# Optimization experiments

Measured on AMD Instinct MI355X. Metric: run time of the kernel, lower is better.

The kernel has to match this reference:

```python
import math
import jax, jax.numpy as jnp
import numpy as np

jax.config.update("jax_enable_x64", True)

P_PRIME = 1000003            # prime modulus; p-1 = 2*3*166667
N_FACTORS = (2, 3, 166667)   # prime factors of p-1 (for primitive-root search)
B, NPATCH, L, K, DIM = 4, 784, 9, 16, 28  # batch, patches/sample, patch len, kernels, map dim


def _modpow(base, exp, p, nbits=21):
    """Vectorized modular exponentiation (square-and-multiply), int64, exponents < 2^nbits."""
    shape = jnp.broadcast_shapes(jnp.shape(base), jnp.shape(exp))
    b0 = jnp.broadcast_to(jnp.asarray(base, jnp.int64) % p, shape)
    e = jnp.broadcast_to(jnp.asarray(exp, jnp.int64), shape)
    def body(i, c):
        res, b = c
        res = jnp.where(((e >> i) & 1) == 1, (res * b) % p, res)
        return (res, (b * b) % p)
    res, _ = jax.lax.fori_loop(0, nbits, body, (jnp.ones(shape, jnp.int64), b0))
    return res


def _decrypt_ips(ct0, cts, y, sk_y, g, p):
    """IPFE decrypt + BSGS discrete log. ct0:[B,P] cts:[B,P,L] y:[K,L] sk_y:[K] -> signed ip [K,B,P]."""
    n = p - 1
    powed = _modpow(cts[None], jnp.mod(y, n)[:, None, None, :], p)   # [K,B,P,L]
    num = powed[..., 0]
    for i in range(1, L):                                            # fixed small L=9
        num = (num * powed[..., i]) % p
    denom = _modpow(ct0[None], jnp.mod(sk_y, n)[:, None, None], p)   # [K,B,P]
    val = (num * _modpow(denom, p - 2, p)) % p                       # = g^{<x,y>} mod p (Fermat inverse)
    # baby-step giant-step over group order n
    m = math.isqrt(n - 1) + 1
    n_giant = -(-n // m)
    baby = _modpow(jnp.int64(g), jnp.arange(m, dtype=jnp.int64), p)  # g^j, j in [0,m)
    order = jnp.argsort(baby)
    sb = baby[order]
    ginv_m = _modpow(jnp.int64(g), jnp.int64((n - m) % n), p)        # g^{-m}
    pt = _modpow(ginv_m, jnp.arange(n_giant, dtype=jnp.int64), p)    # g^{-m*i}
    gamma = (val.reshape(-1)[:, None] * pt[None, :]) % p             # [T, n_giant] giant steps
    pos = jnp.clip(jnp.searchsorted(sb, gamma), 0, m - 1)
    hit = sb[pos] == gamma
    cand = jnp.arange(n_giant, dtype=jnp.int64)[None, :] * m + order[pos]
    ip = jnp.min(jnp.where(hit, cand, n), axis=1)                    # unique match: ip = i*m + j
    ip = jnp.where(ip > n // 2, ip - n, ip)                          # signed representative
    return ip.reshape(K, ct0.shape[0], ct0.shape[1])


def _bn(x, g_, b_, m_, v_):
    s = g_ * jax.lax.rsqrt(v_ + 1e-5)
    return (x - m_[None, :, None, None]) * s[None, :, None, None] + b_[None, :, None, None]


def _conv(x, w, b):
    o = jax.lax.conv_general_dilated(x, w, (1, 1), ((1, 1), (1, 1)),
                                     dimension_numbers=("NCHW", "OIHW", "NCHW"))
    return o + b[None, :, None, None]


def _pool(x):
    return jax.lax.reduce_window(x, jnp.array(-jnp.inf, x.dtype), jax.lax.max,
                                 (1, 1, 2, 2), (1, 1, 2, 2), "VALID")


def _forward(ct0, cts, y, sk_y, bias1, bn1_g, bn1_b, bn1_m, bn1_v,
             conv2_w, conv2_b, bn2_g, bn2_b, bn2_m, bn2_v,
             conv3_w, conv3_b, bn3_g, bn3_b, bn3_m, bn3_v,
             fc1_w, fc1_b, fc2_w, fc2_b, g, p):
    ip = _decrypt_ips(ct0, cts, y, sk_y, g, p)                       # [K,B,P] int64
    maps = ip.astype(jnp.float32) / 10000.0 + bias1[:, None, None]   # dequantize + conv1 bias
    feat = jnp.transpose(maps, (1, 0, 2)).reshape(-1, K, DIM, DIM)   # [B,16,28,28]
    feat = _pool(jax.nn.relu(_bn(feat, bn1_g, bn1_b, bn1_m, bn1_v)))
    feat = _pool(jax.nn.relu(_bn(_conv(feat, conv2_w, conv2_b), bn2_g, bn2_b, bn2_m, bn2_v)))
    feat = _pool(jax.nn.relu(_bn(_conv(feat, conv3_w, conv3_b), bn3_g, bn3_b, bn3_m, bn3_v)))
    flat = feat.reshape(feat.shape[0], -1)                           # [B,576]
    h = jax.nn.relu(flat @ fc1_w.T + fc1_b)                          # dropout = identity (eval mode)
    return h @ fc2_w.T + fc2_b                                       # [B,10]


def setup_inputs():
    rng = np.random.default_rng(0)
    p, n = P_PRIME, P_PRIME - 1
    assert all(p % d for d in range(2, math.isqrt(p) + 1))           # p prime
    g = next(gg for gg in range(2, 200)
             if all(pow(gg, n // q, p) != 1 for q in N_FACTORS))      # primitive root mod p
    s = rng.integers(1, n, size=L)                                    # master secret
    pk = [pow(g, int(si), p) for si in s]
    y = rng.integers(-50, 51, size=(K, L)).astype(np.int64)          # round(w*10000)
    x = rng.integers(0, 21, size=(B, NPATCH, L))                     # quantized patch values
    r = rng.integers(1, n, size=(B, NPATCH))
    gx = [pow(g, t, p) for t in range(21)]
    ct0 = np.zeros((B, NPATCH), dtype=np.int64)
    cts = np.zeros((B, NPATCH, L), dtype=np.int64)
    for b in range(B):
        for j in range(NPATCH):
            rr = int(r[b, j])
            ct0[b, j] = pow(g, rr, p)
            for i in range(L):
                cts[b, j, i] = pow(pk[i], rr, p) * gx[x[b, j, i]] % p
    sk_y = np.array([sum(int(s[i]) * int(y[k, i]) for i in range(L)) % n
                     for k in range(K)], dtype=np.int64)
    f32 = lambda a: jnp.asarray(a, jnp.float32)
    def rn(*sh):
        return f32(rng.standard_normal(sh) * 0.1)
    def bnp(c):
        return (f32(1.0 + 0.1 * rng.standard_normal(c)), rn(c), rn(c), f32(rng.random(c) + 0.5))
    bn1_g, bn1_b, bn1_m, bn1_v = bnp(16)
    bn2_g, bn2_b, bn2_m, bn2_v = bnp(32)
    bn3_g, bn3_b, bn3_m, bn3_v = bnp(64)
    return dict(ct0=jnp.asarray(ct0), cts=jnp.asarray(cts),
                y=jnp.asarray(y), sk_y=jnp.asarray(sk_y), bias1=rn(K),
                bn1_g=bn1_g, bn1_b=bn1_b, bn1_m=bn1_m, bn1_v=bn1_v,
                conv2_w=rn(32, 16, 3, 3), conv2_b=rn(32),
                bn2_g=bn2_g, bn2_b=bn2_b, bn2_m=bn2_m, bn2_v=bn2_v,
                conv3_w=rn(64, 32, 3, 3), conv3_b=rn(64),
                bn3_g=bn3_g, bn3_b=bn3_b, bn3_m=bn3_m, bn3_v=bn3_v,
                fc1_w=rn(128, 576), fc1_b=rn(128),
                fc2_w=rn(10, 128), fc2_b=rn(10), g=g, p=p)


def reference(ct0, cts, y, sk_y, bias1, bn1_g, bn1_b, bn1_m, bn1_v,
              conv2_w, conv2_b, bn2_g, bn2_b, bn2_m, bn2_v,
              conv3_w, conv3_b, bn3_g, bn3_b, bn3_m, bn3_v,
              fc1_w, fc1_b, fc2_w, fc2_b, g, p):
    return _forward(ct0, cts, y, sk_y, bias1, bn1_g, bn1_b, bn1_m, bn1_v,
                    conv2_w, conv2_b, bn2_g, bn2_b, bn2_m, bn2_v,
                    conv3_w, conv3_b, bn3_g, bn3_b, bn3_m, bn3_v,
                    fc1_w, fc1_b, fc2_w, fc2_b, g, p)
```

## Files before the change

kernel.cpp:

```cpp
#include <hip/hip_runtime.h>
#include <stdint.h>

#define PRIME 1000003u
#define NORD  1000002u
#define KCH   16
#define BATCH 4
#define NPATCH 784
#define LLEN  9
#define IPMAX 9000
#define TBLN  (2*IPMAX+1)
#define NDEC  (KCH*BATCH*NPATCH)
#define NBLK  196

__device__ __forceinline__ uint32_t mmul(uint32_t a, uint32_t b) {
    uint64_t t = (uint64_t)a * (uint64_t)b;
    uint32_t q = (uint32_t)((t * 2199016ull) >> 41);
    uint32_t r = (uint32_t)t - q * PRIME;
    return (r >= PRIME) ? r - PRIME : r;
}

__device__ __forceinline__ uint32_t mpow(uint32_t base, uint32_t exp) {
    uint32_t r = 1u, b = base;
    while (exp) {
        if (exp & 1u) r = mmul(r, b);
        b = mmul(b, b);
        exp >>= 1;
    }
    return r;
}

__device__ __forceinline__ void cstore(float* p, float v) {
    __hip_atomic_store(p, v, __ATOMIC_RELAXED, __HIP_MEMORY_SCOPE_AGENT);
}
__device__ __forceinline__ float cload(const float* p) {
    return __hip_atomic_load(p, __ATOMIC_RELAXED, __HIP_MEMORY_SCOPE_AGENT);
}

__device__ __forceinline__ void arrive(unsigned* ctr) {
    __syncthreads();
    if (threadIdx.x == 0)
        __hip_atomic_fetch_add(ctr, 1u, __ATOMIC_RELAXED, __HIP_MEMORY_SCOPE_AGENT);
}
__device__ __forceinline__ void wait_ctr(unsigned* ctr, unsigned target) {
    if (threadIdx.x == 0)
        while (__hip_atomic_load(ctr, __ATOMIC_RELAXED, __HIP_MEMORY_SCOPE_AGENT) < target)
            __builtin_amdgcn_s_sleep(2);
    __syncthreads();
}

__global__ void build_table(const int* __restrict__ g_in, int16_t* __restrict__ table,
                            unsigned* __restrict__ ctr) {
    int e = blockIdx.x * blockDim.x + threadIdx.x;
    if (e >= TBLN) return;
    if (e == 0)
        __hip_atomic_store(ctr, 0u, __ATOMIC_RELAXED, __HIP_MEMORY_SCOPE_AGENT);
    int es = e - IPMAX;
    uint32_t exp = (es >= 0) ? (uint32_t)es : (uint32_t)(es + (int)NORD);
    table[mpow((uint32_t)g_in[0], exp)] = (int16_t)es;
}

__global__ void __launch_bounds__(256) fused(
    const int* __restrict__ ct0, const int* __restrict__ cts,
    const int* __restrict__ y, const int* __restrict__ sk_y,
    const float* __restrict__ bias1,
    const float* __restrict__ bn1_g, const float* __restrict__ bn1_b,
    const float* __restrict__ bn1_m, const float* __restrict__ bn1_v,
    const float* __restrict__ conv2_w, const float* __restrict__ conv2_b,
    const float* __restrict__ bn2_g, const float* __restrict__ bn2_b,
    const float* __restrict__ bn2_m, const float* __restrict__ bn2_v,
    const float* __restrict__ conv3_w, const float* __restrict__ conv3_b,
    const float* __restrict__ bn3_g, const float* __restrict__ bn3_b,
    const float* __restrict__ bn3_m, const float* __restrict__ bn3_v,
    const float* __restrict__ fc1_w, const float* __restrict__ fc1_b,
    const float* __restrict__ fc2_w, const float* __restrict__ fc2_b,
    const int16_t* __restrict__ table,
    float* __restrict__ featr, float* __restrict__ s2g, float* __restrict__ s3g,
    float* __restrict__ out, unsigned* __restrict__ ctr) {

    __shared__ union {
        struct { float s1p[16][16][16]; float w[144]; float co[196]; } c2;
        struct { float s2p[32][9][9];  float w[4][288]; float co[4][49]; } c3;
        struct { float s3[576]; float h[128]; } fc;
    } sm;

    const int bid = blockIdx.x;
    const int tid = threadIdx.x;

    {
        int gtid = bid * 256 + tid;
        int k = __builtin_amdgcn_readfirstlane(gtid / (BATCH * NPATCH));
        int r = gtid % (BATCH * NPATCH);
        int b = r / NPATCH;
        int j = r % NPATCH;

        const int* crow = cts + ((b * NPATCH) + j) * LLEN;
        const int* yrow = y + k * LLEN;

        uint32_t c[LLEN];
        int yv[LLEN];
#pragma unroll
        for (int i = 0; i < LLEN; i++) {
            yv[i] = yrow[i];
            c[i]  = (uint32_t)crow[i];
        }

        uint32_t accp = 1u, accn = 1u;
#pragma unroll
        for (int bit = 5; bit >= 0; bit--) {
            accp = mmul(accp, accp);
            accn = mmul(accn, accn);
#pragma unroll
            for (int i = 0; i < LLEN; i++) {
                int yi = yv[i];
                int ay = (yi > 0) ? yi : -yi;
                if ((ay >> bit) & 1) {
                    if (yi > 0) accp = mmul(accp, c[i]);
                    else        accn = mmul(accn, c[i]);
                }
            }
        }

        uint32_t den = mpow((uint32_t)ct0[b * NPATCH + j], (uint32_t)sk_y[k]);
        den = mmul(den, accn);
        uint32_t val = mmul(accp, mpow(den, PRIME - 2u));

        int ip = (int)table[val];

        float sc = bn1_g[k] * rsqrtf(bn1_v[k] + 1e-5f);
        float shf = (bias1[k] - bn1_m[k]) * sc + bn1_b[k];
        float v_ = fmaf((float)ip, sc * 1e-4f, shf);
        cstore(&featr[((b * KCH) + k) * NPATCH + j], fmaxf(v_, 0.0f));
    }

    arrive(ctr);
    if (bid >= 128) return;
    wait_ctr(ctr, NBLK);

    {
        const int b  = bid >> 5;
        const int oc = bid & 31;

        for (int i = tid; i < 16 * 16 * 16; i += 256)
            ((float*)sm.c2.s1p)[i] = 0.0f;
        if (tid < 144) sm.c2.w[tid] = conv2_w[oc * 144 + tid];
        __syncthreads();
        for (int i = tid; i < 16 * 196; i += 256) {
            int ic = i / 196, pos = i % 196;
            int yy = pos / 14, xx = pos % 14;
            const float* fp = featr + ((b * 16 + ic) * 784) + (2 * yy) * 28 + 2 * xx;
            sm.c2.s1p[ic][yy + 1][xx + 1] =
                fmaxf(fmaxf(cload(fp + 0), cload(fp + 1)),
                      fmaxf(cload(fp + 28), cload(fp + 29)));
        }
        __syncthreads();

        if (tid < 196) {
            int oh = tid / 14, ow = tid % 14;
            float a0 = 0.0f, a1 = 0.0f, a2 = 0.0f;
#pragma unroll
            for (int ic = 0; ic < 16; ic++) {
                const float* wp = &sm.c2.w[ic * 9];
                const float* sp = &sm.c2.s1p[ic][oh][ow];
                a0 = fmaf(sp[0],  wp[0], fmaf(sp[1],  wp[1], fmaf(sp[2],  wp[2], a0)));
                a1 = fmaf(sp[16], wp[3], fmaf(sp[17], wp[4], fmaf(sp[18], wp[5], a1)));
                a2 = fmaf(sp[32], wp[6], fmaf(sp[33], wp[7], fmaf(sp[34], wp[8], a2)));
            }
            float sc = bn2_g[oc] * rsqrtf(bn2_v[oc] + 1e-5f);
            float shf = bn2_b[oc] - bn2_m[oc] * sc;
            sm.c2.co[tid] = fmaxf((a0 + a1 + a2 + conv2_b[oc]) * sc + shf, 0.0f);
        }
        __syncthreads();

        if (tid < 49) {
            int oh = tid / 7, ow = tid % 7;
            const float* c0 = &sm.c2.co[(2 * oh) * 14 + 2 * ow];
            cstore(&s2g[((b * 32 + oc) * 49) + tid],
                   fmaxf(fmaxf(c0[0], c0[1]), fmaxf(c0[14], c0[15])));
        }
    }

    arrive(ctr);
    if (bid >= 64) return;
    wait_ctr(ctr, NBLK + 128);

    {
        const int b = bid >> 4, ocg = bid & 15;

        for (int i = tid; i < 32 * 81; i += 256)
            ((float*)sm.c3.s2p)[i] = 0.0f;
        for (int i = tid; i < 4 * 288; i += 256) {
            int w2 = i / 288, rr = i % 288;
            sm.c3.w[w2][rr] = conv3_w[(ocg * 4 + w2) * 288 + rr];
        }
        __syncthreads();
        for (int i = tid; i < 32 * 49; i += 256) {
            int ic = i / 49, pos = i % 49;
            sm.c3.s2p[ic][pos / 7 + 1][pos % 7 + 1] = cload(&s2g[((b * 32 + ic) * 49) + pos]);
        }
        __syncthreads();

        const int wid = tid >> 6, lane = tid & 63;
        if (lane < 49) {
            int oh = lane / 7, ow = lane % 7;
            float a0 = 0.0f, a1 = 0.0f, a2 = 0.0f;
#pragma unroll
            for (int ic = 0; ic < 32; ic++) {
                const float* wp = &sm.c3.w[wid][ic * 9];
                const float* sp = &sm.c3.s2p[ic][oh][ow];
                a0 = fmaf(sp[0],  wp[0], fmaf(sp[1],  wp[1], fmaf(sp[2],  wp[2], a0)));
                a1 = fmaf(sp[9],  wp[3], fmaf(sp[10], wp[4], fmaf(sp[11], wp[5], a1)));
                a2 = fmaf(sp[18], wp[6], fmaf(sp[19], wp[7], fmaf(sp[20], wp[8], a2)));
            }
            int oc = ocg * 4 + wid;
            float sc = bn3_g[oc] * rsqrtf(bn3_v[oc] + 1e-5f);
            float shf = bn3_b[oc] - bn3_m[oc] * sc;
            sm.c3.co[wid][lane] = fmaxf((a0 + a1 + a2 + conv3_b[oc]) * sc + shf, 0.0f);
        }
        __syncthreads();

        if (tid < 36) {
            int w2 = tid / 9, p = tid % 9;
            int oh = p / 3, ow = p % 3;
            const float* c0 = &sm.c3.co[w2][(2 * oh) * 7 + 2 * ow];
            cstore(&s3g[b * 576 + (ocg * 4 + w2) * 9 + p],
                   fmaxf(fmaxf(c0[0], c0[1]), fmaxf(c0[7], c0[8])));
        }
    }

    arrive(ctr);
    if (bid >= BATCH) return;
    wait_ctr(ctr, NBLK + 128 + 64);

    {
        const int b = bid;
        for (int i = tid; i < 576; i += 256) sm.fc.s3[i] = cload(&s3g[b * 576 + i]);
        __syncthreads();

        const int wid = tid >> 6, lane = tid & 63;
        for (int oo = 0; oo < 32; oo++) {
            int o = wid * 32 + oo;
            const float* w = fc1_w + o * 576;
            float acc = 0.0f;
#pragma unroll
            for (int jj = 0; jj < 9; jj++)
                acc = fmaf(sm.fc.s3[jj * 64 + lane], w[jj * 64 + lane], acc);
#pragma unroll
            for (int off = 32; off; off >>= 1) acc += __shfl_down(acc, off);
            if (lane == 0) sm.fc.h[o] = fmaxf(acc + fc1_b[o], 0.0f);
        }
        __syncthreads();

        for (int o = wid; o < 10; o += 4) {
            const float* w = fc2_w + o * 128;
            float acc = fmaf(sm.fc.h[lane], w[lane], 0.0f);
            acc = fmaf(sm.fc.h[64 + lane], w[64 + lane], acc);
#pragma unroll
            for (int off = 32; off; off >>= 1) acc += __shfl_down(acc, off);
            if (lane == 0) out[b * 10 + o] = acc + fc2_b[o];
        }
    }
}

extern "C" void kernel_launch(void* const* d_in, const int* in_sizes, int n_in,
                              void* d_out, int out_size, void* d_ws, size_t ws_size,
                              hipStream_t stream) {
    const int*   ct0    = (const int*)d_in[0];
    const int*   cts    = (const int*)d_in[1];
    const int*   y      = (const int*)d_in[2];
    const int*   sk_y   = (const int*)d_in[3];
    const float* bias1  = (const float*)d_in[4];
    const float* bn1_g  = (const float*)d_in[5];
    const float* bn1_b  = (const float*)d_in[6];
    const float* bn1_m  = (const float*)d_in[7];
    const float* bn1_v  = (const float*)d_in[8];
    const float* conv2_w = (const float*)d_in[9];
    const float* conv2_b = (const float*)d_in[10];
    const float* bn2_g  = (const float*)d_in[11];
    const float* bn2_b  = (const float*)d_in[12];
    const float* bn2_m  = (const float*)d_in[13];
    const float* bn2_v  = (const float*)d_in[14];
    const float* conv3_w = (const float*)d_in[15];
    const float* conv3_b = (const float*)d_in[16];
    const float* bn3_g  = (const float*)d_in[17];
    const float* bn3_b  = (const float*)d_in[18];
    const float* bn3_m  = (const float*)d_in[19];
    const float* bn3_v  = (const float*)d_in[20];
    const float* fc1_w  = (const float*)d_in[21];
    const float* fc1_b  = (const float*)d_in[22];
    const float* fc2_w  = (const float*)d_in[23];
    const float* fc2_b  = (const float*)d_in[24];
    const int*   g_in   = (const int*)d_in[25];
    float* out = (float*)d_out;

    char* ws = (char*)d_ws;
    int16_t*  table = (int16_t*)ws;
    unsigned* ctr   = (unsigned*)(ws + 2000064);
    float* featr = (float*)(ws + 2000128);
    float* s2g   = (float*)(ws + 2200832);
    float* s3g   = (float*)(ws + 2225920);

    build_table<<<(TBLN + 255) / 256, 256, 0, stream>>>(g_in, table, ctr);

    fused<<<NBLK, 256, 0, stream>>>(
        ct0, cts, y, sk_y, bias1, bn1_g, bn1_b, bn1_m, bn1_v,
        conv2_w, conv2_b, bn2_g, bn2_b, bn2_m, bn2_v,
        conv3_w, conv3_b, bn3_g, bn3_b, bn3_m, bn3_v,
        fc1_w, fc1_b, fc2_w, fc2_b, table, featr, s2g, s3g, out, ctr);
}
```

Measured before the change: 158.5 us.

## Restructure fused kernel work split, fuse pool1, shard barrier counters, parallelize fc1

Changes the fused kernel to 128 blocks of 832 threads. 64 blocks each decrypt one (kernel, batch) plane and max-pool it in shared memory before writing a pooled map, so conv2 reads pre-pooled data. The single global barrier counter becomes eight padded counters that are summed when polled, to reduce atomic contention. fc1 now runs as its own stage across 64 blocks, adding another grid barrier, and fc2 runs one output per wave. The trade-off is fewer, larger blocks, with only half the grid active during decryption.

Measured after the change: 131.2 us. 1.21x faster.

```diff
diff --git a/kernel.cpp b/kernel.cpp
--- a/kernel.cpp
+++ b/kernel.cpp
@@ -9,8 +9,15 @@
 #define LLEN  9
 #define IPMAX 9000
 #define TBLN  (2*IPMAX+1)
-#define NDEC  (KCH*BATCH*NPATCH)
-#define NBLK  196
+#define NBLK  128
+#define ABLK  64
+#define TPB   832
+
+#define CTR_OFF   2000064
+#define POOL_OFF  2001024
+#define S2G_OFF   2051200
+#define S3G_OFF   2076288
+#define HG_OFF    2085504
 
 __device__ __forceinline__ uint32_t mmul(uint32_t a, uint32_t b) {
     uint64_t t = (uint64_t)a * (uint64_t)b;
@@ -36,30 +43,39 @@
     return __hip_atomic_load(p, __ATOMIC_RELAXED, __HIP_MEMORY_SCOPE_AGENT);
 }
 
-__device__ __forceinline__ void arrive(unsigned* ctr) {
+__device__ __forceinline__ void arrive8(unsigned* ctrs, int bid) {
     __syncthreads();
     if (threadIdx.x == 0)
-        __hip_atomic_fetch_add(ctr, 1u, __ATOMIC_RELAXED, __HIP_MEMORY_SCOPE_AGENT);
-}
-__device__ __forceinline__ void wait_ctr(unsigned* ctr, unsigned target) {
-    if (threadIdx.x == 0)
-        while (__hip_atomic_load(ctr, __ATOMIC_RELAXED, __HIP_MEMORY_SCOPE_AGENT) < target)
-            __builtin_amdgcn_s_sleep(2);
+        __hip_atomic_fetch_add(&ctrs[(bid & 7) * 16], 1u,
+                               __ATOMIC_RELAXED, __HIP_MEMORY_SCOPE_AGENT);
+}
+__device__ __forceinline__ void wait8(unsigned* ctrs, unsigned target) {
+    if (threadIdx.x == 0) {
+        for (;;) {
+            unsigned s = 0;
+#pragma unroll
+            for (int i = 0; i < 8; i++)
+                s += __hip_atomic_load(&ctrs[i * 16],
+                                       __ATOMIC_RELAXED, __HIP_MEMORY_SCOPE_AGENT);
+            if (s >= target) break;
+            __builtin_amdgcn_s_sleep(8);
+        }
+    }
     __syncthreads();
 }
 
 __global__ void build_table(const int* __restrict__ g_in, int16_t* __restrict__ table,
-                            unsigned* __restrict__ ctr) {
+                            unsigned* __restrict__ ctrs) {
     int e = blockIdx.x * blockDim.x + threadIdx.x;
     if (e >= TBLN) return;
-    if (e == 0)
-        __hip_atomic_store(ctr, 0u, __ATOMIC_RELAXED, __HIP_MEMORY_SCOPE_AGENT);
+    if (e < 8)
+        __hip_atomic_store(&ctrs[e * 16], 0u, __ATOMIC_RELAXED, __HIP_MEMORY_SCOPE_AGENT);
     int es = e - IPMAX;
     uint32_t exp = (es >= 0) ? (uint32_t)es : (uint32_t)(es + (int)NORD);
     table[mpow((uint32_t)g_in[0], exp)] = (int16_t)es;
 }
 
-__global__ void __launch_bounds__(256) fused(
+__global__ void __launch_bounds__(TPB) fused(
     const int* __restrict__ ct0, const int* __restrict__ cts,
     const int* __restrict__ y, const int* __restrict__ sk_y,
     const float* __restrict__ bias1,
@@ -74,83 +90,85 @@
     const float* __restrict__ fc1_w, const float* __restrict__ fc1_b,
     const float* __restrict__ fc2_w, const float* __restrict__ fc2_b,
     const int16_t* __restrict__ table,
-    float* __restrict__ featr, float* __restrict__ s2g, float* __restrict__ s3g,
-    float* __restrict__ out, unsigned* __restrict__ ctr) {
+    float* __restrict__ pooled, float* __restrict__ s2g, float* __restrict__ s3g,
+    float* __restrict__ hg, float* __restrict__ out, unsigned* __restrict__ ctrs) {
 
     __shared__ union {
+        float raw[784];
         struct { float s1p[16][16][16]; float w[144]; float co[196]; } c2;
         struct { float s2p[32][9][9];  float w[4][288]; float co[4][49]; } c3;
-        struct { float s3[576]; float h[128]; } fc;
+        struct { float s3[576]; } d1;
+        struct { float h[128]; } d2;
     } sm;
 
     const int bid = blockIdx.x;
     const int tid = threadIdx.x;
 
-    {
-        int gtid = bid * 256 + tid;
-        int k = __builtin_amdgcn_readfirstlane(gtid / (BATCH * NPATCH));
-        int r = gtid % (BATCH * NPATCH);
-        int b = r / NPATCH;
-        int j = r % NPATCH;
-
-        const int* crow = cts + ((b * NPATCH) + j) * LLEN;
+    if (bid < ABLK) {
+        const int k = bid & 15, b = bid >> 4;
         const int* yrow = y + k * LLEN;
-
-        uint32_t c[LLEN];
         int yv[LLEN];
 #pragma unroll
-        for (int i = 0; i < LLEN; i++) {
-            yv[i] = yrow[i];
-            c[i]  = (uint32_t)crow[i];
-        }
-
-        uint32_t accp = 1u, accn = 1u;
-#pragma unroll
-        for (int bit = 5; bit >= 0; bit--) {
-            accp = mmul(accp, accp);
-            accn = mmul(accn, accn);
-#pragma unroll
-            for (int i = 0; i < LLEN; i++) {
-                int yi = yv[i];
-                int ay = (yi > 0) ? yi : -yi;
-                if ((ay >> bit) & 1) {
-                    if (yi > 0) accp = mmul(accp, c[i]);
-                    else        accn = mmul(accn, c[i]);
+        for (int i = 0; i < LLEN; i++) yv[i] = yrow[i];
+        const uint32_t sk = (uint32_t)sk_y[k];
+        const float sc  = bn1_g[k] * rsqrtf(bn1_v[k] + 1e-5f);
+        const float shf = (bias1[k] - bn1_m[k]) * sc + bn1_b[k];
+
+        if (tid < NPATCH) {
+            const int j = tid;
+            const int* crow = cts + ((b * NPATCH) + j) * LLEN;
+            uint32_t c[LLEN];
+#pragma unroll
+            for (int i = 0; i < LLEN; i++) c[i] = (uint32_t)crow[i];
+
+            uint32_t accp = 1u, accn = 1u;
+#pragma unroll
+            for (int bit = 5; bit >= 0; bit--) {
+                accp = mmul(accp, accp);
+                accn = mmul(accn, accn);
+#pragma unroll
+                for (int i = 0; i < LLEN; i++) {
+                    int yi = yv[i];
+                    int ay = (yi > 0) ? yi : -yi;
+                    if ((ay >> bit) & 1) {
+                        if (yi > 0) accp = mmul(accp, c[i]);
+                        else        accn = mmul(accn, c[i]);
+                    }
                 }
             }
-        }
-
-        uint32_t den = mpow((uint32_t)ct0[b * NPATCH + j], (uint32_t)sk_y[k]);
-        den = mmul(den, accn);
-        uint32_t val = mmul(accp, mpow(den, PRIME - 2u));
-
-        int ip = (int)table[val];
-
-        float sc = bn1_g[k] * rsqrtf(bn1_v[k] + 1e-5f);
-        float shf = (bias1[k] - bn1_m[k]) * sc + bn1_b[k];
-        float v_ = fmaf((float)ip, sc * 1e-4f, shf);
-        cstore(&featr[((b * KCH) + k) * NPATCH + j], fmaxf(v_, 0.0f));
-    }
-
-    arrive(ctr);
-    if (bid >= 128) return;
-    wait_ctr(ctr, NBLK);
+
+            uint32_t den = mpow((uint32_t)ct0[b * NPATCH + j], sk);
+            den = mmul(den, accn);
+            uint32_t val = mmul(accp, mpow(den, PRIME - 2u));
+
+            int ip = (int)table[val];
+            float v_ = fmaf((float)ip, sc * 1e-4f, shf);
+            sm.raw[j] = fmaxf(v_, 0.0f);
+        }
+        __syncthreads();
+        if (tid < 196) {
+            int py = tid / 14, px = tid % 14;
+            const float* r0 = &sm.raw[(2 * py) * 28 + 2 * px];
+            float m = fmaxf(fmaxf(r0[0], r0[1]), fmaxf(r0[28], r0[29]));
+            cstore(&pooled[((b * KCH) + k) * 196 + tid], m);
+        }
+        arrive8(ctrs, bid);
+    }
+
+    wait8(ctrs, ABLK);
 
     {
         const int b  = bid >> 5;
         const int oc = bid & 31;
 
-        for (int i = tid; i < 16 * 16 * 16; i += 256)
+        for (int i = tid; i < 16 * 16 * 16; i += TPB)
             ((float*)sm.c2.s1p)[i] = 0.0f;
         if (tid < 144) sm.c2.w[tid] = conv2_w[oc * 144 + tid];
         __syncthreads();
-        for (int i = tid; i < 16 * 196; i += 256) {
+        for (int i = tid; i < 16 * 196; i += TPB) {
             int ic = i / 196, pos = i % 196;
             int yy = pos / 14, xx = pos % 14;
-            const float* fp = featr + ((b * 16 + ic) * 784) + (2 * yy) * 28 + 2 * xx;
-            sm.c2.s1p[ic][yy + 1][xx + 1] =
-                fmaxf(fmaxf(cload(fp + 0), cload(fp + 1)),
-                      fmaxf(cload(fp + 28), cload(fp + 29)));
+            sm.c2.s1p[ic][yy + 1][xx + 1] = cload(&pooled[((b * KCH) + ic) * 196 + pos]);
         }
         __syncthreads();
 
@@ -179,28 +197,28 @@
         }
     }
 
-    arrive(ctr);
+    arrive8(ctrs, bid);
     if (bid >= 64) return;
-    wait_ctr(ctr, NBLK + 128);
+    wait8(ctrs, ABLK + NBLK);
 
     {
         const int b = bid >> 4, ocg = bid & 15;
 
-        for (int i = tid; i < 32 * 81; i += 256)
+        for (int i = tid; i < 32 * 81; i += TPB)
             ((float*)sm.c3.s2p)[i] = 0.0f;
-        for (int i = tid; i < 4 * 288; i += 256) {
+        for (int i = tid; i < 4 * 288; i += TPB) {
             int w2 = i / 288, rr = i % 288;
             sm.c3.w[w2][rr] = conv3_w[(ocg * 4 + w2) * 288 + rr];
         }
         __syncthreads();
-        for (int i = tid; i < 32 * 49; i += 256) {
+        for (int i = tid; i < 32 * 49; i += TPB) {
             int ic = i / 49, pos = i % 49;
             sm.c3.s2p[ic][pos / 7 + 1][pos % 7 + 1] = cload(&s2g[((b * 32 + ic) * 49) + pos]);
         }
         __syncthreads();
 
         const int wid = tid >> 6, lane = tid & 63;
-        if (lane < 49) {
+        if (wid < 4 && lane < 49) {
             int oh = lane / 7, ow = lane % 7;
             float a0 = 0.0f, a1 = 0.0f, a2 = 0.0f;
 #pragma unroll
@@ -227,36 +245,45 @@
         }
     }
 
-    arrive(ctr);
+    arrive8(ctrs, bid);
+    wait8(ctrs, ABLK + NBLK + 64);
+
+    {
+        const int b = bid >> 4, og = bid & 15;
+        for (int i = tid; i < 576; i += TPB) sm.d1.s3[i] = cload(&s3g[b * 576 + i]);
+        __syncthreads();
+
+        const int wid = tid >> 6, lane = tid & 63;
+        if (wid < 8) {
+            int o = og * 8 + wid;
+            const float* w = fc1_w + o * 576;
+            float acc = 0.0f;
+#pragma unroll
+            for (int jj = 0; jj < 9; jj++)
+                acc = fmaf(sm.d1.s3[jj * 64 + lane], w[jj * 64 + lane], acc);
+#pragma unroll
+            for (int off = 32; off; off >>= 1) acc += __shfl_down(acc, off);
+            if (lane == 0) cstore(&hg[b * 128 + o], fmaxf(acc + fc1_b[o], 0.0f));
+        }
+    }
+
+    arrive8(ctrs, bid);
     if (bid >= BATCH) return;
-    wait_ctr(ctr, NBLK + 128 + 64);
+    wait8(ctrs, ABLK + NBLK + 64 + 64);
 
     {
         const int b = bid;
-        for (int i = tid; i < 576; i += 256) sm.fc.s3[i] = cload(&s3g[b * 576 + i]);
+        if (tid < 128) sm.d2.h[tid] = cload(&hg[b * 128 + tid]);
         __syncthreads();
 
         const int wid = tid >> 6, lane = tid & 63;
-        for (int oo = 0; oo < 32; oo++) {
-            int o = wid * 32 + oo;
-            const float* w = fc1_w + o * 576;
-            float acc = 0.0f;
-#pragma unroll
-            for (int jj = 0; jj < 9; jj++)
-                acc = fmaf(sm.fc.s3[jj * 64 + lane], w[jj * 64 + lane], acc);
+        if (wid < 10) {
+            const float* w = fc2_w + wid * 128;
+            float acc = fmaf(sm.d2.h[lane], w[lane], 0.0f);
+            acc = fmaf(sm.d2.h[64 + lane], w[64 + lane], acc);
 #pragma unroll
             for (int off = 32; off; off >>= 1) acc += __shfl_down(acc, off);
-            if (lane == 0) sm.fc.h[o] = fmaxf(acc + fc1_b[o], 0.0f);
-        }
-        __syncthreads();
-
-        for (int o = wid; o < 10; o += 4) {
-            const float* w = fc2_w + o * 128;
-            float acc = fmaf(sm.fc.h[lane], w[lane], 0.0f);
-            acc = fmaf(sm.fc.h[64 + lane], w[64 + lane], acc);
-#pragma unroll
-            for (int off = 32; off; off >>= 1) acc += __shfl_down(acc, off);
-            if (lane == 0) out[b * 10 + o] = acc + fc2_b[o];
+            if (lane == 0) out[b * 10 + wid] = acc + fc2_b[wid];
         }
     }
 }
@@ -293,17 +320,18 @@
     float* out = (float*)d_out;
 
     char* ws = (char*)d_ws;
-    int16_t*  table = (int16_t*)ws;
-    unsigned* ctr   = (unsigned*)(ws + 2000064);
-    float* featr = (float*)(ws + 2000128);
-    float* s2g   = (float*)(ws + 2200832);
-    float* s3g   = (float*)(ws + 2225920);
-
-    build_table<<<(TBLN + 255) / 256, 256, 0, stream>>>(g_in, table, ctr);
-
-    fused<<<NBLK, 256, 0, stream>>>(
+    int16_t*  table  = (int16_t*)ws;
+    unsigned* ctrs   = (unsigned*)(ws + CTR_OFF);
+    float* pooled = (float*)(ws + POOL_OFF);
+    float* s2g    = (float*)(ws + S2G_OFF);
+    float* s3g    = (float*)(ws + S3G_OFF);
+    float* hg     = (float*)(ws + HG_OFF);
+
+    build_table<<<(TBLN + 255) / 256, 256, 0, stream>>>(g_in, table, ctrs);
+
+    fused<<<NBLK, TPB, 0, stream>>>(
         ct0, cts, y, sk_y, bias1, bn1_g, bn1_b, bn1_m, bn1_v,
         conv2_w, conv2_b, bn2_g, bn2_b, bn2_m, bn2_v,
         conv3_w, conv3_b, bn3_g, bn3_b, bn3_m, bn3_v,
-        fc1_w, fc1_b, fc2_w, fc2_b, table, featr, s2g, s3g, out, ctr);
-}
+        fc1_w, fc1_b, fc2_w, fc2_b, table, pooled, s2g, s3g, hg, out, ctrs);
+}
```
